# Kernel tuning notes

Hardware: AMD Instinct MI355X
Metric: run time of the kernel (lower is better)

## Reference

```python
import jax, jax.numpy as jnp
import numpy as np

V, E, H = 100000, 300, 256          # pretrained vectors, emb_dim, rep_dim
B, QLEN, DOC, S = 32, 32, 2048, 64  # batch, max_query_len, max_doc_len, max_num_sent
L = DOC // S                        # sentence length (lengths sum exactly to DOC)
VOCAB = V + 2                       # + extra token + padding idx


def _uniform(k, shape, scale):
    return jax.random.uniform(k, shape, jnp.float32, -scale, scale)


def setup_inputs() -> dict:
    key = jax.random.key(0)
    ks = jax.random.split(key, 16)
    s = 1.0 / np.sqrt(H)  # PyTorch GRU default init scale
    return {
        "queries": jax.random.randint(ks[0], (B, QLEN), 0, V),
        "query_lengths": jax.random.randint(ks[1], (B,), QLEN // 2, QLEN + 1).astype(jnp.int32),
        "docs": jax.random.randint(ks[2], (B, DOC), 0, V),
        "sentence_lengths": jnp.full((B, S), L, dtype=jnp.int32),
        "emb": jax.random.normal(ks[3], (VOCAB, E), jnp.float32) * 0.1,
        "q_wih": _uniform(ks[4], (3 * H, E), s), "q_whh": _uniform(ks[5], (3 * H, H), s),
        "q_bih": _uniform(ks[6], (3 * H,), s), "q_bhh": _uniform(ks[7], (3 * H,), s),
        "f_wih": _uniform(ks[8], (3 * H, E), s), "f_whh": _uniform(ks[9], (3 * H, H), s),
        "f_bih": _uniform(ks[10], (3 * H,), s), "f_bhh": _uniform(ks[11], (3 * H,), s),
        "b_wih": _uniform(ks[12], (3 * H, E), s), "b_whh": _uniform(ks[13], (3 * H, H), s),
        "b_bih": _uniform(ks[14], (3 * H,), s), "b_bhh": _uniform(ks[15], (3 * H,), s),
    }


def _gru(x, wih, whh, bih, bhh, reverse=False):
    # x: (B, T, E) -> hidden states (B, T, H); PyTorch GRU cell equations.
    xg = jnp.einsum('bte,ge->btg', x, wih) + bih  # (B, T, 3H) input projections

    def step(h, xt):
        gh = h @ whh.T + bhh
        ir, iz, inn = jnp.split(xt, 3, axis=-1)
        hr, hz, hn = jnp.split(gh, 3, axis=-1)
        r = jax.nn.sigmoid(ir + hr)
        z = jax.nn.sigmoid(iz + hz)
        n = jnp.tanh(inn + r * hn)
        hnew = (1.0 - z) * n + z * h
        return hnew, hnew

    h0 = jnp.zeros((x.shape[0], whh.shape[1]), x.dtype)
    _, hs = jax.lax.scan(step, h0, jnp.swapaxes(xg, 0, 1), reverse=reverse)
    return jnp.swapaxes(hs, 0, 1)


def reference(queries, query_lengths, docs, sentence_lengths, emb,
              q_wih, q_whh, q_bih, q_bhh,
              f_wih, f_whh, f_bih, f_bhh,
              b_wih, b_whh, b_bih, b_bhh):
    q_emb = emb[queries]  # (B, QLEN, E)
    d_emb = emb[docs]     # (B, DOC, E)

    # Ragged per-sentence mean pooling (_get_facts) as one segment-mean per doc.
    def seg_mean(xb, lens):
        ids = jnp.repeat(jnp.arange(S), lens, total_repeat_length=DOC)
        sums = jax.ops.segment_sum(xb, ids, num_segments=S)
        return sums / jnp.maximum(lens, 1)[:, None].astype(xb.dtype)

    facts = jax.vmap(seg_mean)(d_emb, sentence_lengths)  # (B, S, E)

    # Question GRU: hidden state at the last valid token (pack_padded semantics).
    q_hs = _gru(q_emb, q_wih, q_whh, q_bih, q_bhh)
    q_rep = q_hs[jnp.arange(B), query_lengths - 1][:, None, :]  # (B, 1, H)

    # Input fusion: bidirectional GRU over facts, fwd + bwd halves summed (dropout off / eval).
    f_out = (_gru(facts, f_wih, f_whh, f_bih, f_bhh)
             + _gru(facts, b_wih, b_whh, b_bih, b_bhh, reverse=True))  # (B, S, H)

    num_facts = jnp.sum(sentence_lengths > 0, axis=1)
    return q_rep, f_out, num_facts
```

## Files before the change

### kernel.cpp

```cpp
#include <hip/hip_runtime.h>

#define Bn   32
#define QL   32
#define DOCn 2048
#define Sn   64
#define En   300
#define Hn   256

typedef short bf16x8 __attribute__((ext_vector_type(8)));
typedef short s16x4  __attribute__((ext_vector_type(4)));
typedef float f32x4  __attribute__((ext_vector_type(4)));

static __device__ __forceinline__ float b2f(short s){
  unsigned int u = ((unsigned int)(unsigned short)s) << 16;
  float f; __builtin_memcpy(&f, &u, 4); return f;
}
static __device__ __forceinline__ short f2b(float f){
  unsigned int u; __builtin_memcpy(&u, &f, 4);
  u = u + 0x7fffu + ((u >> 16) & 1u);
  return (short)(u >> 16);
}
static __device__ __forceinline__ float sigm(float x){ return 1.0f/(1.0f+__expf(-x)); }
static __device__ __forceinline__ float tanhx(float x){ return 1.0f - 2.0f/(__expf(2.0f*x)+1.0f); }
static __device__ __forceinline__ f32x4 mfma16(bf16x8 a, bf16x8 b, f32x4 c){
  return __builtin_amdgcn_mfma_f32_16x16x32_bf16(a, b, c, 0, 0, 0);
}
static __device__ __forceinline__ void bar_lgkm(){
  asm volatile("s_waitcnt lgkmcnt(0)\n\ts_barrier" ::: "memory");
}

__global__ __launch_bounds__(256) void k_facts(
    const int* __restrict__ docs, const int* __restrict__ slens,
    const float* __restrict__ emb, short* __restrict__ facts)
{
  __shared__ int pref[2*Sn];
  const int blk = blockIdx.x;
  const int b = blk >> 6, s = blk & 63;
  const int tid = threadIdx.x;
  if (tid < Sn){
    const int v = slens[b*Sn + tid];
    int x = v;
#pragma unroll
    for (int d = 1; d < 64; d <<= 1){
      const int y = __shfl_up(x, d, 64);
      if (tid >= d) x += y;
    }
    pref[tid] = x - v;
    pref[Sn + tid] = v;
  }
  __syncthreads();
  const int off = pref[s];
  const int len = pref[Sn + s];
  const int e0 = tid;
  float a0 = 0.f, a1 = 0.f;
  const int* dtok = docs + b*DOCn + off;
  int tk = (len > 0) ? dtok[0] : 0;
  for (int l = 0; l < len; ++l){
    const int tkn = (l + 1 < len) ? dtok[l+1] : 0;
    const float* row = emb + (long)tk*En;
    a0 += row[e0];
    if (e0 + 256 < En) a1 += row[e0+256];
    tk = tkn;
  }
  const float inv = 1.0f / (float)(len > 0 ? len : 1);
  short* frow = facts + ((long)b*Sn + s)*En;
  frow[e0] = f2b(a0*inv);
  if (e0 + 256 < En) frow[e0+256] = f2b(a1*inv);
}

__global__ __launch_bounds__(256) void k_xg_q(
    const int* __restrict__ queries, const float* __restrict__ emb,
    const float* __restrict__ wih, const float* __restrict__ bih,
    short* __restrict__ xg)
{
  __shared__ alignas(16) short Al[2][64][40];
  const int bm = blockIdx.x, bn = blockIdx.y;
  const int tid = threadIdx.x;
  const int l = tid & 63, w = tid >> 6;
  const int wm = w & 1, wn = w >> 1;
  const int l15 = l & 15, lq = l >> 4;

  bf16x8 bfr[2][10];
#pragma unroll
  for (int nt = 0; nt < 2; ++nt){
    const int g = bn*64 + wn*32 + nt*16 + l15;
    const float* wr = wih + (long)g*En;
#pragma unroll
    for (int kk = 0; kk < 10; ++kk){
      const int k0 = kk*32 + lq*8;
      bf16x8 v;
      if (k0 + 7 < En){
        const f32x4 f0 = *(const f32x4*)(wr + k0);
        const f32x4 f1 = *(const f32x4*)(wr + k0 + 4);
#pragma unroll
        for (int j = 0; j < 4; ++j){ v[j] = f2b(f0[j]); v[4+j] = f2b(f1[j]); }
      } else {
#pragma unroll
        for (int j = 0; j < 8; ++j){ const int k = k0 + j; v[j] = (k < En) ? f2b(wr[k]) : (short)0; }
      }
      bfr[nt][kk] = v;
    }
  }

  const int arow = l;
  const int ak8  = w*8;
  const int tok  = queries[bm*64 + arow];
  const float* asrc = emb + (long)tok*En;

  float ar[8];
#define LDA_Q(KK) do{ const int k0_ = (KK)*32 + ak8; \
    if (k0_ + 7 < En){ const f32x4 f0_ = *(const f32x4*)(asrc+k0_), f1_ = *(const f32x4*)(asrc+k0_+4); \
      ar[0]=f0_[0];ar[1]=f0_[1];ar[2]=f0_[2];ar[3]=f0_[3];ar[4]=f1_[0];ar[5]=f1_[1];ar[6]=f1_[2];ar[7]=f1_[3]; } \
    else { _Pragma("unroll") for (int j=0;j<8;++j){ const int k_=k0_+j; ar[j] = (k_<En)? asrc[k_] : 0.f; } } }while(0)
#define STA_Q(BUF) do{ s16x4 s0_ = (s16x4){f2b(ar[0]),f2b(ar[1]),f2b(ar[2]),f2b(ar[3])}; \
    s16x4 s1_ = (s16x4){f2b(ar[4]),f2b(ar[5]),f2b(ar[6]),f2b(ar[7])}; \
    *(s16x4*)&Al[BUF][arow][ak8] = s0_; *(s16x4*)&Al[BUF][arow][ak8+4] = s1_; }while(0)

  LDA_Q(0); STA_Q(0);
  __syncthreads();

  f32x4 acc[2][2] = {};
#pragma unroll
  for (int kk = 0; kk < 10; ++kk){
    if (kk < 9) LDA_Q(kk+1);
#pragma unroll
    for (int mt = 0; mt < 2; ++mt){
      bf16x8 a = *(const bf16x8*)&Al[kk&1][wm*32 + mt*16 + l15][lq*8];
      acc[mt][0] = mfma16(a, bfr[0][kk], acc[mt][0]);
      acc[mt][1] = mfma16(a, bfr[1][kk], acc[mt][1]);
    }
    if (kk < 9) STA_Q((kk+1)&1);
    __syncthreads();
  }
#undef LDA_Q
#undef STA_Q

#pragma unroll
  for (int nt = 0; nt < 2; ++nt){
    const int cc = bn*64 + wn*32 + nt*16 + l15;
    const float bias = bih[cc];
#pragma unroll
    for (int mt = 0; mt < 2; ++mt){
      const int r0 = bm*64 + wm*32 + mt*16 + lq*4;
#pragma unroll
      for (int p = 0; p < 4; ++p)
        xg[(long)(r0+p)*768 + cc] = f2b(acc[mt][nt][p] + bias);
    }
  }
}

__global__ __launch_bounds__(256) void k_xg_fb(
    const short* __restrict__ facts,
    const float* __restrict__ f_wih, const float* __restrict__ f_bih,
    const float* __restrict__ b_wih, const float* __restrict__ b_bih,
    short* __restrict__ f_xg, short* __restrict__ b_xg)
{
  __shared__ alignas(16) short Al[2][64][40];
  const float* wih = blockIdx.z ? b_wih : f_wih;
  const float* bih = blockIdx.z ? b_bih : f_bih;
  short*       xg  = blockIdx.z ? b_xg  : f_xg;

  const int bm = blockIdx.x, bn = blockIdx.y;
  const int tid = threadIdx.x;
  const int l = tid & 63, w = tid >> 6;
  const int wm = w & 1, wn = w >> 1;
  const int l15 = l & 15, lq = l >> 4;

  bf16x8 bfr[2][10];
#pragma unroll
  for (int nt = 0; nt < 2; ++nt){
    const int g = bn*64 + wn*32 + nt*16 + l15;
    const float* wr = wih + (long)g*En;
#pragma unroll
    for (int kk = 0; kk < 10; ++kk){
      const int k0 = kk*32 + lq*8;
      bf16x8 v;
      if (k0 + 7 < En){
        const f32x4 f0 = *(const f32x4*)(wr + k0);
        const f32x4 f1 = *(const f32x4*)(wr + k0 + 4);
#pragma unroll
        for (int j = 0; j < 4; ++j){ v[j] = f2b(f0[j]); v[4+j] = f2b(f1[j]); }
      } else {
#pragma unroll
        for (int j = 0; j < 8; ++j){ const int k = k0 + j; v[j] = (k < En) ? f2b(wr[k]) : (short)0; }
      }
      bfr[nt][kk] = v;
    }
  }

  const int arow = l;
  const int ak8  = w*8;
  const short* asrc = facts + (long)(bm*64 + arow)*En;

  s16x4 a0_, a1_;
#define LDA_F(KK) do{ const int k0_ = (KK)*32 + ak8; \
    if (k0_ + 7 < En){ a0_ = *(const s16x4*)(asrc+k0_); a1_ = *(const s16x4*)(asrc+k0_+4); } \
    else { _Pragma("unroll") for (int j=0;j<4;++j){ const int ka_=k0_+j, kb_=k0_+4+j; \
      a0_[j] = (ka_<En)? asrc[ka_] : (short)0; a1_[j] = (kb_<En)? asrc[kb_] : (short)0; } } }while(0)
#define STA_F(BUF) do{ *(s16x4*)&Al[BUF][arow][ak8] = a0_; *(s16x4*)&Al[BUF][arow][ak8+4] = a1_; }while(0)

  LDA_F(0); STA_F(0);
  __syncthreads();

  f32x4 acc[2][2] = {};
#pragma unroll
  for (int kk = 0; kk < 10; ++kk){
    if (kk < 9) LDA_F(kk+1);
#pragma unroll
    for (int mt = 0; mt < 2; ++mt){
      bf16x8 a = *(const bf16x8*)&Al[kk&1][wm*32 + mt*16 + l15][lq*8];
      acc[mt][0] = mfma16(a, bfr[0][kk], acc[mt][0]);
      acc[mt][1] = mfma16(a, bfr[1][kk], acc[mt][1]);
    }
    if (kk < 9) STA_F((kk+1)&1);
    __syncthreads();
  }
#undef LDA_F
#undef STA_F

#pragma unroll
  for (int nt = 0; nt < 2; ++nt){
    const int cc = bn*64 + wn*32 + nt*16 + l15;
    const float bias = bih[cc];
#pragma unroll
    for (int mt = 0; mt < 2; ++mt){
      const int r0 = bm*64 + wm*32 + mt*16 + lq*4;
#pragma unroll
      for (int p = 0; p < 4; ++p)
        xg[(long)(r0+p)*768 + cc] = f2b(acc[mt][nt][p] + bias);
    }
  }
}

__global__ __launch_bounds__(1024) void k_gru(
    const short* __restrict__ q_xg, const short* __restrict__ f_xg,
    const short* __restrict__ b_xg,
    const float* __restrict__ q_whh, const float* __restrict__ q_bhh,
    const float* __restrict__ f_whh, const float* __restrict__ f_bhh,
    const float* __restrict__ b_whh, const float* __restrict__ b_bhh,
    const int* __restrict__ qlens,
    short* __restrict__ f_hs, short* __restrict__ b_hs,
    float* __restrict__ dout)
{
  __shared__ alignas(16) short hl[2*4224];
  __shared__ alignas(16) short wl[6*1024*8];

  const int gru = blockIdx.x >> 1;
  const int mh  = blockIdx.x & 1;
  const int tid = threadIdx.x;
  const int l = tid & 63, w = tid >> 6;
  const int l15 = l & 15, lq = l >> 4;

  const float* whh = (gru == 0) ? q_whh : (gru == 1) ? f_whh : b_whh;
  const float* bhh = (gru == 0) ? q_bhh : (gru == 1) ? f_bhh : b_bhh;
  const short* xg  = (gru == 0) ? q_xg  : (gru == 1) ? f_xg  : b_xg;
  const int T = (gru == 0) ? QL : Sn;

  const int c = w*16 + l15;

  bf16x8 wf[3][6];
  float bias[3];
#pragma unroll
  for (int gi = 0; gi < 3; ++gi){
    const int g = gi*256 + c;
    const float* wr = whh + (long)g*Hn;
#pragma unroll
    for (int kk = 0; kk < 8; ++kk){
      const f32x4 f0 = *(const f32x4*)(wr + kk*32 + lq*8);
      const f32x4 f1 = *(const f32x4*)(wr + kk*32 + lq*8 + 4);
      bf16x8 v;
#pragma unroll
      for (int j = 0; j < 4; ++j){ v[j] = f2b(f0[j]); v[4+j] = f2b(f1[j]); }
      if (kk < 6) wf[gi][kk] = v;
      else *(bf16x8*)&wl[((gi*2 + (kk-6))*1024 + tid)*8] = v;
    }
    bias[gi] = bhh[g];
  }

  for (int i = tid; i < 4224; i += 1024) hl[i] = 0;

  float hreg[4] = {};
  int qlen_m[4];
#pragma unroll
  for (int p = 0; p < 4; ++p) qlen_m[p] = qlens[mh*16 + lq*4 + p];

  const int rowT768 = T*768;
  const short* xbase = xg + (long)(mh*16 + lq*4)*rowT768 + c;
  short* hsb = ((gru == 1) ? f_hs : b_hs) + (long)(mh*16 + lq*4)*(Sn*Hn) + c;
  float* qdst = dout + (mh*16 + lq*4)*Hn + c;

  __syncthreads();

  short pre[12];
#define TOF(TT) ((gru == 2) ? (T - 1 - (TT)) : (TT))
#define LOADP(TI) do{ const int _to = (TI)*768; \
  _Pragma("unroll") for (int p = 0; p < 4; ++p){ \
    const short* _xr = xbase + p*rowT768 + _to; \
    pre[p*3+0] = _xr[0]; pre[p*3+1] = _xr[256]; pre[p*3+2] = _xr[512]; } }while(0)

#define GRU_STEP(TT, DOM, HIN, HOUT) do{ \
    f32x4 acc[3]; \
    _Pragma("unroll") for (int gi = 0; gi < 3; ++gi){ const float bv = bias[gi]; acc[gi] = (f32x4){bv,bv,bv,bv}; } \
    if (DOM){ \
      _Pragma("unroll") for (int kk = 0; kk < 6; ++kk){ \
        const bf16x8 a = *(const bf16x8*)&(HIN)[l15*264 + kk*32 + lq*8]; \
        acc[0] = mfma16(a, wf[0][kk], acc[0]); \
        acc[1] = mfma16(a, wf[1][kk], acc[1]); \
        acc[2] = mfma16(a, wf[2][kk], acc[2]); \
      } \
      _Pragma("unroll") for (int kk = 6; kk < 8; ++kk){ \
        const bf16x8 a  = *(const bf16x8*)&(HIN)[l15*264 + kk*32 + lq*8]; \
        const bf16x8 w0 = *(const bf16x8*)&wl[((0*2 + (kk-6))*1024 + tid)*8]; \
        const bf16x8 w1 = *(const bf16x8*)&wl[((1*2 + (kk-6))*1024 + tid)*8]; \
        const bf16x8 w2 = *(const bf16x8*)&wl[((2*2 + (kk-6))*1024 + tid)*8]; \
        acc[0] = mfma16(a, w0, acc[0]); \
        acc[1] = mfma16(a, w1, acc[1]); \
        acc[2] = mfma16(a, w2, acc[2]); \
      } \
    } \
    const int t_ = TOF(TT); \
    _Pragma("unroll") for (int p = 0; p < 4; ++p){ \
      const int r_ = lq*4 + p; \
      const float ir = b2f(pre[p*3+0]), iz = b2f(pre[p*3+1]), in_ = b2f(pre[p*3+2]); \
      const float rr = sigm(ir + acc[0][p]); \
      const float zz = sigm(iz + acc[1][p]); \
      const float nn = tanhx(in_ + rr*acc[2][p]); \
      const float hn = (1.0f - zz)*nn + zz*hreg[p]; \
      hreg[p] = hn; \
      (HOUT)[r_*264 + c] = f2b(hn); \
      if (gru == 0){ if (t_ == qlen_m[p] - 1) qdst[p*Hn] = hn; } \
      else { hsb[p*(Sn*Hn) + t_*Hn] = f2b(hn); } \
    } \
  }while(0)

  short* h0 = hl;
  short* h1 = hl + 4224;

  LOADP(TOF(0));
  GRU_STEP(0, 0, h0, h1);
  LOADP(TOF(1));
  bar_lgkm();
  GRU_STEP(1, 1, h1, h0);
  LOADP(TOF(2));
  bar_lgkm();

  for (int tt = 2; tt < T; tt += 2){
    GRU_STEP(tt, 1, h0, h1);
    LOADP(TOF(tt+1));
    bar_lgkm();
    GRU_STEP(tt+1, 1, h1, h0);
    if (tt + 2 < T) LOADP(TOF(tt+2));
    bar_lgkm();
  }
#undef TOF
#undef LOADP
#undef GRU_STEP
}

__global__ __launch_bounds__(256) void k_combine(
    const short* __restrict__ f_hs, const short* __restrict__ b_hs,
    const int* __restrict__ slens, float* __restrict__ dout)
{
  const int i4 = (blockIdx.x*256 + threadIdx.x) * 4;
  const s16x4 fv = *(const s16x4*)(f_hs + i4);
  const s16x4 bv = *(const s16x4*)(b_hs + i4);
  f32x4 o;
#pragma unroll
  for (int j = 0; j < 4; ++j) o[j] = b2f(fv[j]) + b2f(bv[j]);
  *(f32x4*)(dout + Bn*Hn + i4) = o;
  if (blockIdx.x == 0 && threadIdx.x < Bn){
    const int* ls = slens + threadIdx.x*Sn;
    int cnt = 0;
#pragma unroll
    for (int s = 0; s < Sn; ++s) cnt += (ls[s] > 0) ? 1 : 0;
    dout[Bn*Hn + Bn*Sn*Hn + threadIdx.x] = (float)cnt;
  }
}

extern "C" void kernel_launch(void* const* d_in, const int* in_sizes, int n_in,
                              void* d_out, int out_size, void* d_ws, size_t ws_size,
                              hipStream_t stream)
{
  const int*   queries = (const int*)d_in[0];
  const int*   qlens   = (const int*)d_in[1];
  const int*   docs    = (const int*)d_in[2];
  const int*   slens   = (const int*)d_in[3];
  const float* emb     = (const float*)d_in[4];
  const float* q_wih   = (const float*)d_in[5];
  const float* q_whh   = (const float*)d_in[6];
  const float* q_bih   = (const float*)d_in[7];
  const float* q_bhh   = (const float*)d_in[8];
  const float* f_wih   = (const float*)d_in[9];
  const float* f_whh   = (const float*)d_in[10];
  const float* f_bih   = (const float*)d_in[11];
  const float* f_bhh   = (const float*)d_in[12];
  const float* b_wih   = (const float*)d_in[13];
  const float* b_whh   = (const float*)d_in[14];
  const float* b_bih   = (const float*)d_in[15];
  const float* b_bhh   = (const float*)d_in[16];

  char* wsb = (char*)d_ws;
  short* f_xg  = (short*)(wsb);
  short* b_xg  = (short*)(wsb +  3145728);
  short* q_xg  = (short*)(wsb +  6291456);
  short* facts = (short*)(wsb +  7864320);
  short* f_hs  = (short*)(wsb +  9093120);
  short* b_hs  = (short*)(wsb + 10141696);

  float* dout = (float*)d_out;

  k_facts<<<dim3(Bn*Sn), 256, 0, stream>>>(docs, slens, emb, facts);
  k_xg_q <<<dim3(16, 12), 256, 0, stream>>>(queries, emb, q_wih, q_bih, q_xg);
  k_xg_fb<<<dim3(32, 12, 2), 256, 0, stream>>>(facts, f_wih, f_bih, b_wih, b_bih, f_xg, b_xg);
  k_gru  <<<dim3(6), 1024, 0, stream>>>(q_xg, f_xg, b_xg, q_whh, q_bhh,
                                        f_whh, f_bhh, b_whh, b_bhh,
                                        qlens, f_hs, b_hs, dout);
  k_combine<<<dim3(512), 256, 0, stream>>>(f_hs, b_hs, slens, dout);
}
```

Baseline: 493.4 us.

## Interleave gate projections time-major so GRU prefetches one vector per row

The input-projection kernels now write their outputs in a time-major layout with the three gates interleaved per hidden unit (stride 4). This lets each recurrent step fetch r/z/n for a row with one 8-byte load instead of three scalar loads. The GRU loop double-buffers these preloads two steps ahead and uses scheduling barriers. One extra recurrent weight fragment is moved from registers to LDS, and hidden-state history is stored time-major, with the combine kernel remapping it back to batch-major output. Facts and f_hs share the same workspace offset, which relies on facts being dead before the GRU writes f_hs. The h-buffer zero-init was dropped, which is safe only because step 0 skips the matmul.

```diff
diff --git a/kernel.cpp b/kernel.cpp
--- a/kernel.cpp
+++ b/kernel.cpp
@@ -71,7 +71,7 @@
 __global__ __launch_bounds__(256) void k_xg_q(
     const int* __restrict__ queries, const float* __restrict__ emb,
     const float* __restrict__ wih, const float* __restrict__ bih,
-    short* __restrict__ xg)
+    short* __restrict__ xgi)
 {
   __shared__ alignas(16) short Al[2][64][40];
   const int bm = blockIdx.x, bn = blockIdx.y;
@@ -137,14 +137,17 @@
 
 #pragma unroll
   for (int nt = 0; nt < 2; ++nt){
-    const int cc = bn*64 + wn*32 + nt*16 + l15;
-    const float bias = bih[cc];
+    const int cg = bn*64 + wn*32 + nt*16 + l15;
+    const float bias = bih[cg];
+    const int gate = cg >> 8, hc = cg & 255;
 #pragma unroll
     for (int mt = 0; mt < 2; ++mt){
       const int r0 = bm*64 + wm*32 + mt*16 + lq*4;
 #pragma unroll
-      for (int p = 0; p < 4; ++p)
-        xg[(long)(r0+p)*768 + cc] = f2b(acc[mt][nt][p] + bias);
+      for (int p = 0; p < 4; ++p){
+        const int r = r0 + p;
+        xgi[((long)((r & 31)*32 + (r >> 5)))*1024 + hc*4 + gate] = f2b(acc[mt][nt][p] + bias);
+      }
     }
   }
 }
@@ -153,12 +156,12 @@
     const short* __restrict__ facts,
     const float* __restrict__ f_wih, const float* __restrict__ f_bih,
     const float* __restrict__ b_wih, const float* __restrict__ b_bih,
-    short* __restrict__ f_xg, short* __restrict__ b_xg)
+    short* __restrict__ f_xgi, short* __restrict__ b_xgi)
 {
   __shared__ alignas(16) short Al[2][64][40];
   const float* wih = blockIdx.z ? b_wih : f_wih;
   const float* bih = blockIdx.z ? b_bih : f_bih;
-  short*       xg  = blockIdx.z ? b_xg  : f_xg;
+  short*       xgi = blockIdx.z ? b_xgi : f_xgi;
 
   const int bm = blockIdx.x, bn = blockIdx.y;
   const int tid = threadIdx.x;
@@ -220,14 +223,17 @@
 
 #pragma unroll
   for (int nt = 0; nt < 2; ++nt){
-    const int cc = bn*64 + wn*32 + nt*16 + l15;
-    const float bias = bih[cc];
+    const int cg = bn*64 + wn*32 + nt*16 + l15;
+    const float bias = bih[cg];
+    const int gate = cg >> 8, hc = cg & 255;
 #pragma unroll
     for (int mt = 0; mt < 2; ++mt){
       const int r0 = bm*64 + wm*32 + mt*16 + lq*4;
 #pragma unroll
-      for (int p = 0; p < 4; ++p)
-        xg[(long)(r0+p)*768 + cc] = f2b(acc[mt][nt][p] + bias);
+      for (int p = 0; p < 4; ++p){
+        const int r = r0 + p;
+        xgi[((long)((r & 63)*32 + (r >> 6)))*1024 + hc*4 + gate] = f2b(acc[mt][nt][p] + bias);
+      }
     }
   }
 }
@@ -242,8 +248,8 @@
     short* __restrict__ f_hs, short* __restrict__ b_hs,
     float* __restrict__ dout)
 {
-  __shared__ alignas(16) short hl[2*4224];
-  __shared__ alignas(16) short wl[6*1024*8];
+  __shared__ alignas(16) short hl[2*16*264];
+  __shared__ alignas(16) short wl[7*1024*8];
 
   const int gru = blockIdx.x >> 1;
   const int mh  = blockIdx.x & 1;
@@ -253,7 +259,7 @@
 
   const float* whh = (gru == 0) ? q_whh : (gru == 1) ? f_whh : b_whh;
   const float* bhh = (gru == 0) ? q_bhh : (gru == 1) ? f_bhh : b_bhh;
-  const short* xg  = (gru == 0) ? q_xg  : (gru == 1) ? f_xg  : b_xg;
+  const short* xgp = (gru == 0) ? q_xg  : (gru == 1) ? f_xg  : b_xg;
   const int T = (gru == 0) ? QL : Sn;
 
   const int c = w*16 + l15;
@@ -271,85 +277,101 @@
       bf16x8 v;
 #pragma unroll
       for (int j = 0; j < 4; ++j){ v[j] = f2b(f0[j]); v[4+j] = f2b(f1[j]); }
-      if (kk < 6) wf[gi][kk] = v;
-      else *(bf16x8*)&wl[((gi*2 + (kk-6))*1024 + tid)*8] = v;
+      if (kk < 5 || (kk == 5 && gi < 2)) wf[gi][kk] = v;
+      else if (kk == 5)                  *(bf16x8*)&wl[(6*1024 + tid)*8] = v;
+      else                               *(bf16x8*)&wl[(((kk-6)*3 + gi)*1024 + tid)*8] = v;
     }
     bias[gi] = bhh[g];
   }
-
-  for (int i = tid; i < 4224; i += 1024) hl[i] = 0;
 
   float hreg[4] = {};
   int qlen_m[4];
 #pragma unroll
-  for (int p = 0; p < 4; ++p) qlen_m[p] = qlens[mh*16 + lq*4 + p];
-
-  const int rowT768 = T*768;
-  const short* xbase = xg + (long)(mh*16 + lq*4)*rowT768 + c;
-  short* hsb = ((gru == 1) ? f_hs : b_hs) + (long)(mh*16 + lq*4)*(Sn*Hn) + c;
+  for (int p = 0; p < 4; ++p) qlen_m[p] = (gru == 0) ? qlens[mh*16 + lq*4 + p] : -1;
+
+  const int vo  = (mh*16 + lq*4)*1024 + c*4;
+  const int svo = (mh*16 + lq*4)*256 + c;
+  short* hsp = (gru == 1) ? f_hs : b_hs;
   float* qdst = dout + (mh*16 + lq*4)*Hn + c;
 
-  __syncthreads();
-
-  short pre[12];
+  s16x4 preA[4], preB[4];
+
 #define TOF(TT) ((gru == 2) ? (T - 1 - (TT)) : (TT))
-#define LOADP(TI) do{ const int _to = (TI)*768; \
-  _Pragma("unroll") for (int p = 0; p < 4; ++p){ \
-    const short* _xr = xbase + p*rowT768 + _to; \
-    pre[p*3+0] = _xr[0]; pre[p*3+1] = _xr[256]; pre[p*3+2] = _xr[512]; } }while(0)
-
-#define GRU_STEP(TT, DOM, HIN, HOUT) do{ \
-    f32x4 acc[3]; \
-    _Pragma("unroll") for (int gi = 0; gi < 3; ++gi){ const float bv = bias[gi]; acc[gi] = (f32x4){bv,bv,bv,bv}; } \
+#define LOADP(PRE, TI) do{ const short* sb_ = xgp + (long)(TI)*32768 + vo; \
+    PRE[0] = *(const s16x4*)(sb_); \
+    PRE[1] = *(const s16x4*)(sb_ + 1024); \
+    PRE[2] = *(const s16x4*)(sb_ + 2048); \
+    PRE[3] = *(const s16x4*)(sb_ + 3072); }while(0)
+
+#define GRU_STEP(TT, DOM, HIN, HOUT, PRE) do{ \
+    f32x4 acc0 = (f32x4){bias[0],bias[0],bias[0],bias[0]}; \
+    f32x4 acc1 = (f32x4){bias[1],bias[1],bias[1],bias[1]}; \
+    f32x4 acc2 = (f32x4){bias[2],bias[2],bias[2],bias[2]}; \
     if (DOM){ \
-      _Pragma("unroll") for (int kk = 0; kk < 6; ++kk){ \
+      _Pragma("unroll") for (int kk = 0; kk < 5; ++kk){ \
         const bf16x8 a = *(const bf16x8*)&(HIN)[l15*264 + kk*32 + lq*8]; \
-        acc[0] = mfma16(a, wf[0][kk], acc[0]); \
-        acc[1] = mfma16(a, wf[1][kk], acc[1]); \
-        acc[2] = mfma16(a, wf[2][kk], acc[2]); \
+        acc0 = mfma16(a, wf[0][kk], acc0); \
+        acc1 = mfma16(a, wf[1][kk], acc1); \
+        acc2 = mfma16(a, wf[2][kk], acc2); \
       } \
-      _Pragma("unroll") for (int kk = 6; kk < 8; ++kk){ \
-        const bf16x8 a  = *(const bf16x8*)&(HIN)[l15*264 + kk*32 + lq*8]; \
-        const bf16x8 w0 = *(const bf16x8*)&wl[((0*2 + (kk-6))*1024 + tid)*8]; \
-        const bf16x8 w1 = *(const bf16x8*)&wl[((1*2 + (kk-6))*1024 + tid)*8]; \
-        const bf16x8 w2 = *(const bf16x8*)&wl[((2*2 + (kk-6))*1024 + tid)*8]; \
-        acc[0] = mfma16(a, w0, acc[0]); \
-        acc[1] = mfma16(a, w1, acc[1]); \
-        acc[2] = mfma16(a, w2, acc[2]); \
-      } \
+      { const bf16x8 a = *(const bf16x8*)&(HIN)[l15*264 + 5*32 + lq*8]; \
+        const bf16x8 w2 = *(const bf16x8*)&wl[(6*1024 + tid)*8]; \
+        acc0 = mfma16(a, wf[0][5], acc0); \
+        acc1 = mfma16(a, wf[1][5], acc1); \
+        acc2 = mfma16(a, w2, acc2); } \
+      { const bf16x8 a = *(const bf16x8*)&(HIN)[l15*264 + 6*32 + lq*8]; \
+        const bf16x8 w0 = *(const bf16x8*)&wl[(0*1024 + tid)*8]; \
+        const bf16x8 w1 = *(const bf16x8*)&wl[(1*1024 + tid)*8]; \
+        const bf16x8 w2 = *(const bf16x8*)&wl[(2*1024 + tid)*8]; \
+        acc0 = mfma16(a, w0, acc0); \
+        acc1 = mfma16(a, w1, acc1); \
+        acc2 = mfma16(a, w2, acc2); } \
+      { const bf16x8 a = *(const bf16x8*)&(HIN)[l15*264 + 7*32 + lq*8]; \
+        const bf16x8 w0 = *(const bf16x8*)&wl[(3*1024 + tid)*8]; \
+        const bf16x8 w1 = *(const bf16x8*)&wl[(4*1024 + tid)*8]; \
+        const bf16x8 w2 = *(const bf16x8*)&wl[(5*1024 + tid)*8]; \
+        acc0 = mfma16(a, w0, acc0); \
+        acc1 = mfma16(a, w1, acc1); \
+        acc2 = mfma16(a, w2, acc2); } \
     } \
     const int t_ = TOF(TT); \
+    short* hst = hsp + (long)t_*8192 + svo; \
     _Pragma("unroll") for (int p = 0; p < 4; ++p){ \
-      const int r_ = lq*4 + p; \
-      const float ir = b2f(pre[p*3+0]), iz = b2f(pre[p*3+1]), in_ = b2f(pre[p*3+2]); \
-      const float rr = sigm(ir + acc[0][p]); \
-      const float zz = sigm(iz + acc[1][p]); \
-      const float nn = tanhx(in_ + rr*acc[2][p]); \
+      const float ir = b2f(PRE[p][0]), iz = b2f(PRE[p][1]), in_ = b2f(PRE[p][2]); \
+      const float rr = sigm(ir + acc0[p]); \
+      const float zz = sigm(iz + acc1[p]); \
+      const float nn = tanhx(in_ + rr*acc2[p]); \
       const float hn = (1.0f - zz)*nn + zz*hreg[p]; \
       hreg[p] = hn; \
-      (HOUT)[r_*264 + c] = f2b(hn); \
+      (HOUT)[(lq*4 + p)*264 + c] = f2b(hn); \
       if (gru == 0){ if (t_ == qlen_m[p] - 1) qdst[p*Hn] = hn; } \
-      else { hsb[p*(Sn*Hn) + t_*Hn] = f2b(hn); } \
+      else { hst[p*256] = f2b(hn); } \
     } \
   }while(0)
 
   short* h0 = hl;
   short* h1 = hl + 4224;
 
-  LOADP(TOF(0));
-  GRU_STEP(0, 0, h0, h1);
-  LOADP(TOF(1));
+  LOADP(preA, TOF(0));
+  LOADP(preB, TOF(1));
+  __builtin_amdgcn_sched_barrier(0);
+  GRU_STEP(0, 0, h1, h0, preA);
   bar_lgkm();
-  GRU_STEP(1, 1, h1, h0);
-  LOADP(TOF(2));
+  LOADP(preA, TOF(2));
+  __builtin_amdgcn_sched_barrier(0);
+  GRU_STEP(1, 1, h0, h1, preB);
   bar_lgkm();
 
   for (int tt = 2; tt < T; tt += 2){
-    GRU_STEP(tt, 1, h0, h1);
-    LOADP(TOF(tt+1));
+    const int tiB = (tt+1 < T) ? (tt+1) : (T-1);
+    LOADP(preB, TOF(tiB));
+    __builtin_amdgcn_sched_barrier(0);
+    GRU_STEP(tt, 1, h1, h0, preA);
     bar_lgkm();
-    GRU_STEP(tt+1, 1, h1, h0);
-    if (tt + 2 < T) LOADP(TOF(tt+2));
+    const int tiA = (tt+2 < T) ? (tt+2) : (T-1);
+    LOADP(preA, TOF(tiA));
+    __builtin_amdgcn_sched_barrier(0);
+    GRU_STEP(tt+1, 1, h0, h1, preB);
     bar_lgkm();
   }
 #undef TOF
@@ -364,10 +386,11 @@
   const int i4 = (blockIdx.x*256 + threadIdx.x) * 4;
   const s16x4 fv = *(const s16x4*)(f_hs + i4);
   const s16x4 bv = *(const s16x4*)(b_hs + i4);
+  const int t = i4 >> 13, bb = (i4 >> 8) & 31, cc = i4 & 255;
   f32x4 o;
 #pragma unroll
   for (int j = 0; j < 4; ++j) o[j] = b2f(fv[j]) + b2f(bv[j]);
-  *(f32x4*)(dout + Bn*Hn + i4) = o;
+  *(f32x4*)(dout + Bn*Hn + ((long)bb << 14) + (t << 8) + cc) = o;
   if (blockIdx.x == 0 && threadIdx.x < Bn){
     const int* ls = slens + threadIdx.x*Sn;
     int cnt = 0;
@@ -400,19 +423,19 @@
   const float* b_bhh   = (const float*)d_in[16];
 
   char* wsb = (char*)d_ws;
-  short* f_xg  = (short*)(wsb);
-  short* b_xg  = (short*)(wsb +  3145728);
-  short* q_xg  = (short*)(wsb +  6291456);
-  short* facts = (short*)(wsb +  7864320);
-  short* f_hs  = (short*)(wsb +  9093120);
-  short* b_hs  = (short*)(wsb + 10141696);
+  short* f_xgi = (short*)(wsb);
+  short* b_xgi = (short*)(wsb +  4194304);
+  short* q_xgi = (short*)(wsb +  8388608);
+  short* facts = (short*)(wsb + 10485760);
+  short* f_hs  = (short*)(wsb + 10485760);
+  short* b_hs  = (short*)(wsb + 11714560);
 
   float* dout = (float*)d_out;
 
   k_facts<<<dim3(Bn*Sn), 256, 0, stream>>>(docs, slens, emb, facts);
-  k_xg_q <<<dim3(16, 12), 256, 0, stream>>>(queries, emb, q_wih, q_bih, q_xg);
-  k_xg_fb<<<dim3(32, 12, 2), 256, 0, stream>>>(facts, f_wih, f_bih, b_wih, b_bih, f_xg, b_xg);
-  k_gru  <<<dim3(6), 1024, 0, stream>>>(q_xg, f_xg, b_xg, q_whh, q_bhh,
+  k_xg_q <<<dim3(16, 12), 256, 0, stream>>>(queries, emb, q_wih, q_bih, q_xgi);
+  k_xg_fb<<<dim3(32, 12, 2), 256, 0, stream>>>(facts, f_wih, f_bih, b_wih, b_bih, f_xgi, b_xgi);
+  k_gru  <<<dim3(6), 1024, 0, stream>>>(q_xgi, f_xgi, b_xgi, q_whh, q_bhh,
                                         f_whh, f_bhh, b_whh, b_bhh,
                                         qlens, f_hs, b_hs, dout);
   k_combine<<<dim3(512), 256, 0, stream>>>(f_hs, b_hs, slens, dout);
```

Result: slower. 503.5 us (+2.0%).
